# Optimization experiments

Measured on AMD Instinct MI355X. Metric: run time of the kernel, lower is better.

Reference implementation:

```python
import jax, jax.numpy as jnp
import numpy as np

HEAD_SIZE = 16
HIDDEN = 1024
NEG_INF = -1e9


def setup_inputs() -> dict:
    key = jax.random.key(0)
    ks = jax.random.split(key, 9)
    B, S, H = 2, 2048, HIDDEN
    q = jax.random.normal(ks[0], (B, S, H), dtype=jnp.float32)
    k = jax.random.normal(ks[1], (B, S, H), dtype=jnp.float32)
    v = jax.random.normal(ks[2], (B, S, H), dtype=jnp.float32)
    mask = jnp.ones((B, S), dtype=jnp.int32)
    scale = 1.0 / np.sqrt(H)
    wq = jax.random.normal(ks[3], (H, H), dtype=jnp.float32) * scale
    bq = jnp.zeros((H,), dtype=jnp.float32)
    wk = jax.random.normal(ks[4], (H, H), dtype=jnp.float32) * scale
    bk = jnp.zeros((H,), dtype=jnp.float32)
    wv = jax.random.normal(ks[5], (H, H), dtype=jnp.float32) * scale
    bv = jnp.zeros((H,), dtype=jnp.float32)
    return {"q": q, "k": k, "v": v, "mask": mask,
            "wq": wq, "bq": bq, "wk": wk, "bk": bk, "wv": wv, "bv": bv}


def _split_heads(x):
    # [B, S, H] -> [B, n_heads, S, head_dim]
    B, S, H = x.shape
    return x.reshape(B, S, HEAD_SIZE, H // HEAD_SIZE).transpose(0, 2, 1, 3)


def reference(q, k, v, mask, wq, bq, wk, bk, wv, bv):
    B, S, H = q.shape
    qh = _split_heads(q @ wq + bq)  # [B, nH, S, d]
    kh = _split_heads(k @ wk + bk)
    vh = _split_heads(v @ wv + bv)
    # scores scaled by sqrt(hidden_size) -- faithful to original (not head_dim)
    scores = jnp.einsum('bhqd,bhkd->bhqk', qh, kh) / jnp.sqrt(jnp.float32(H))
    # original: mask[0] of shape [B,S] -> [B,1,S,1], masks query rows
    m = mask.astype(jnp.float32)[:, None, :, None]  # [B,1,S,1]
    scores = scores + NEG_INF * (1.0 - m)
    weights = jax.nn.softmax(scores, axis=-1)
    out = jnp.einsum('bhqk,bhkd->bhqd', weights, vh)  # [B, nH, S, d]
    return out.transpose(0, 2, 1, 3).reshape(B, S, H)
```

## Files before the change

### kernel.cpp

```cpp
#include <hip/hip_runtime.h>
#include <hip/hip_bf16.h>
#include <math.h>

typedef __bf16 bf16_t;
typedef __bf16 bf16x8 __attribute__((ext_vector_type(8)));
typedef __bf16 bf16x4 __attribute__((ext_vector_type(4)));
typedef float floatx4 __attribute__((ext_vector_type(4)));

#define QSCALE 0.045084222f

__device__ __forceinline__ void gload_lds16(const bf16_t* g, bf16_t* l) {
  __builtin_amdgcn_global_load_lds(
      (const __attribute__((address_space(1))) void*)(g),
      (__attribute__((address_space(3))) void*)(l), 16, 0, 0);
}

__device__ __forceinline__ float fast_exp2(float x) {
  float r;
  asm("v_exp_f32 %0, %1" : "=v"(r) : "v"(x));
  return r;
}

__global__ __launch_bounds__(256) void cvt3_k(
    const float* __restrict__ q, const float* __restrict__ k,
    const float* __restrict__ v, bf16_t* __restrict__ xb) {
  const float* src = (blockIdx.y == 0) ? q : (blockIdx.y == 1) ? k : v;
  bf16_t* dst = xb + (size_t)blockIdx.y * 4194304u;
  const int i = (blockIdx.x * 256 + threadIdx.x) * 8;
  float4 f0 = *(const float4*)(src + i);
  float4 f1 = *(const float4*)(src + i + 4);
  bf16x8 hv;
  hv[0] = (bf16_t)f0.x; hv[1] = (bf16_t)f0.y;
  hv[2] = (bf16_t)f0.z; hv[3] = (bf16_t)f0.w;
  hv[4] = (bf16_t)f1.x; hv[5] = (bf16_t)f1.y;
  hv[6] = (bf16_t)f1.z; hv[7] = (bf16_t)f1.w;
  *(bf16x8*)(dst + i) = hv;
}

__global__ __launch_bounds__(256) void transpose3_k(
    const float* __restrict__ wq, const float* __restrict__ wk,
    const float* __restrict__ wv, bf16_t* __restrict__ wt) {
  __shared__ float tile[32][33];
  const float* src = (blockIdx.z == 0) ? wq : (blockIdx.z == 1) ? wk : wv;
  bf16_t* dst = wt + (size_t)blockIdx.z * (1024u * 1024u);
  const int tx = threadIdx.x, ty = threadIdx.y;
  const int x = blockIdx.x * 32 + tx;
  const int y = blockIdx.y * 32 + ty;
#pragma unroll
  for (int i = 0; i < 32; i += 8)
    tile[ty + i][tx] = src[(size_t)(y + i) * 1024 + x];
  __syncthreads();
  const int x2 = blockIdx.y * 32 + tx;
  const int y2 = blockIdx.x * 32 + ty;
#pragma unroll
  for (int i = 0; i < 32; i += 8)
    dst[(size_t)(y2 + i) * 1024 + x2] = (bf16_t)tile[tx][ty + i];
}

__global__ __launch_bounds__(256) void qkv_gemm_k(
    const bf16_t* __restrict__ xb3, const bf16_t* __restrict__ wt3,
    const float* __restrict__ bq, const float* __restrict__ bk,
    const float* __restrict__ bv, bf16_t* __restrict__ Qh,
    bf16_t* __restrict__ Kh, bf16_t* __restrict__ Vt) {
  const int proj = blockIdx.z;
  const bf16_t* X = xb3 + (size_t)proj * 4194304u;
  const bf16_t* Wt = wt3 + (size_t)proj * 1048576u;
  const float* bias = (proj == 0) ? bq : (proj == 1) ? bk : bv;

  __shared__ __align__(16) bf16_t As[128 * 64];
  __shared__ __align__(16) bf16_t Bs[128 * 64];

  const int t = threadIdx.x;
  const int lane = t & 63;
  const int w = t >> 6;
  const int wm = (w >> 1) * 64;
  const int wn = (w & 1) * 64;
  const int m0 = blockIdx.x * 128;
  const int n0 = blockIdx.y * 128;
  const int lm = lane & 15;
  const int lq = lane >> 4;

  int srow[4], sg[4];
#pragma unroll
  for (int c = 0; c < 4; ++c) {
    const int E = c * 2048 + t * 8;
    srow[c] = E >> 6;
    sg[c] = (((E >> 3) & 7) ^ (srow[c] & 7)) * 8;
  }

  floatx4 acc[4][4];
#pragma unroll
  for (int i = 0; i < 4; ++i)
#pragma unroll
    for (int j = 0; j < 4; ++j) acc[i][j] = (floatx4){0.f, 0.f, 0.f, 0.f};

  for (int k0 = 0; k0 < 1024; k0 += 64) {
    __syncthreads();
#pragma unroll
    for (int c = 0; c < 4; ++c) {
      const int E = c * 2048 + t * 8;
      gload_lds16(X + (size_t)(m0 + srow[c]) * 1024 + k0 + sg[c], As + E);
      gload_lds16(Wt + (size_t)(n0 + srow[c]) * 1024 + k0 + sg[c], Bs + E);
    }
    __syncthreads();

#pragma unroll
    for (int kc = 0; kc < 2; ++kc) {
      bf16x8 a[4], b[4];
#pragma unroll
      for (int i = 0; i < 4; ++i) {
        const int ch = ((kc * 4 + lq) ^ (lm & 7)) * 8;
        a[i] = *(const bf16x8*)(As + (wm + i * 16 + lm) * 64 + ch);
        b[i] = *(const bf16x8*)(Bs + (wn + i * 16 + lm) * 64 + ch);
      }
      if (proj < 2) {
#pragma unroll
        for (int i = 0; i < 4; ++i)
#pragma unroll
          for (int j = 0; j < 4; ++j)
            acc[i][j] = __builtin_amdgcn_mfma_f32_16x16x32_bf16(b[j], a[i],
                                                               acc[i][j], 0, 0, 0);
      } else {
#pragma unroll
        for (int i = 0; i < 4; ++i)
#pragma unroll
          for (int j = 0; j < 4; ++j)
            acc[i][j] = __builtin_amdgcn_mfma_f32_16x16x32_bf16(a[i], b[j],
                                                               acc[i][j], 0, 0, 0);
      }
    }
  }

  if (proj == 2) {
#pragma unroll
    for (int j = 0; j < 4; ++j) {
      const int gn = n0 + wn + j * 16 + lm;
      const float bval = bias[gn];
      const int h = gn >> 6, d = gn & 63;
#pragma unroll
      for (int i = 0; i < 4; ++i) {
        const int gm = m0 + wm + i * 16 + lq * 4;
        const int bb = gm >> 11, s0 = gm & 2047;
        bf16x4 pk;
#pragma unroll
        for (int ii = 0; ii < 4; ++ii) pk[ii] = (bf16_t)(acc[i][j][ii] + bval);
        *(bf16x4*)(Vt + (((size_t)bb * 16 + h) * 64 + d) * 2048 + s0) = pk;
      }
    }
  } else {
    bf16_t* outp = (proj == 0) ? Qh : Kh;
    const float scale = (proj == 0) ? QSCALE : 1.0f;
#pragma unroll
    for (int j = 0; j < 4; ++j) {
      const int nb = n0 + wn + j * 16 + lq * 4;
      float bs4[4];
#pragma unroll
      for (int ii = 0; ii < 4; ++ii) bs4[ii] = bias[nb + ii];
      const int h = nb >> 6, d0 = nb & 63;
#pragma unroll
      for (int i = 0; i < 4; ++i) {
        const int gm = m0 + wm + i * 16 + lm;
        const int bb = gm >> 11, s = gm & 2047;
        bf16x4 pk;
#pragma unroll
        for (int ii = 0; ii < 4; ++ii)
          pk[ii] = (bf16_t)((acc[i][j][ii] + bs4[ii]) * scale);
        *(bf16x4*)(outp + (((size_t)bb * 16 + h) * 2048 + s) * 64 + d0) = pk;
      }
    }
  }
}

__global__ __launch_bounds__(256) void attn_k(
    const bf16_t* __restrict__ Qh, const bf16_t* __restrict__ Kh,
    const bf16_t* __restrict__ Vt, float* __restrict__ out) {
  __shared__ __align__(16) bf16_t Ks[128 * 64];
  __shared__ __align__(16) bf16_t Vs[64 * 128];
  __shared__ __align__(16) bf16_t Ps[4][32 * 128];

  const int t = threadIdx.x;
  const int lane = t & 63;
  const int w = t >> 6;
  const int lm = lane & 15;
  const int lq = lane >> 4;
  const int b = blockIdx.x >> 4, h = blockIdx.x & 15;
  const int q0 = blockIdx.y * 128;
  const size_t bh = (size_t)b * 16 + h;
  const bf16_t* Qb = Qh + bh * (2048 * 64);
  const bf16_t* Kb = Kh + bh * (2048 * 64);
  const bf16_t* Vb = Vt + bh * (64 * 2048);

  bf16x8 qf[2][2];
#pragma unroll
  for (int im = 0; im < 2; ++im)
#pragma unroll
    for (int kc = 0; kc < 2; ++kc)
      qf[im][kc] = *(const bf16x8*)(Qb +
          (size_t)(q0 + w * 32 + im * 16 + lm) * 64 + kc * 32 + lq * 8);

  float lsum[2] = {0.f, 0.f};
  floatx4 accO[2][4];
#pragma unroll
  for (int im = 0; im < 2; ++im)
#pragma unroll
    for (int jd = 0; jd < 4; ++jd) accO[im][jd] = (floatx4){0.f, 0.f, 0.f, 0.f};

  bf16x8 kv[8];

#define LOAD_KV(kt)                                                          \
  {                                                                          \
    _Pragma("unroll") for (int c = 0; c < 4; ++c) {                          \
      const int e = c * 2048 + t * 8;                                        \
      const int key = e >> 6, gk = ((e >> 3) & 7) ^ (key & 7);               \
      kv[c] = *(const bf16x8*)(Kb + (size_t)((kt) + key) * 64 + gk * 8);     \
      const int vr = e >> 7, gv = ((e >> 3) & 15) ^ (vr & 15);               \
      kv[4 + c] = *(const bf16x8*)(Vb + (size_t)vr * 2048 + (kt) + gv * 8);  \
    }                                                                        \
  }

  LOAD_KV(0);

  for (int kt = 0; kt < 2048; kt += 128) {
    __syncthreads();
#pragma unroll
    for (int c = 0; c < 4; ++c) {
      const int e = c * 2048 + t * 8;
      *(bf16x8*)(Ks + e) = kv[c];
      *(bf16x8*)(Vs + e) = kv[4 + c];
    }
    __syncthreads();

    if (kt + 128 < 2048) LOAD_KV(kt + 128);

    floatx4 accS[2][8];
#pragma unroll
    for (int jn = 0; jn < 8; ++jn) {
      const int krow = jn * 16 + lm;
      const bf16x8 k0 = *(const bf16x8*)(Ks + krow * 64 + ((lq) ^ (lm & 7)) * 8);
      const bf16x8 k1 = *(const bf16x8*)(Ks + krow * 64 + ((4 + lq) ^ (lm & 7)) * 8);
#pragma unroll
      for (int im = 0; im < 2; ++im) {
        floatx4 z = {0.f, 0.f, 0.f, 0.f};
        z = __builtin_amdgcn_mfma_f32_16x16x32_bf16(k0, qf[im][0], z, 0, 0, 0);
        z = __builtin_amdgcn_mfma_f32_16x16x32_bf16(k1, qf[im][1], z, 0, 0, 0);
        accS[im][jn] = z;
      }
    }

#pragma unroll
    for (int im = 0; im < 2; ++im) {
      const int pr = im * 16 + lm;
#pragma unroll
      for (int jn = 0; jn < 8; ++jn) {
        bf16x4 pk;
#pragma unroll
        for (int ii = 0; ii < 4; ++ii) {
          const float p = fast_exp2(accS[im][jn][ii]);
          lsum[im] += p;
          pk[ii] = (bf16_t)p;
        }
        const int c2 = ((jn * 2) + (lq >> 1)) ^ lm;
        *(bf16x4*)(Ps[w] + pr * 128 + c2 * 8 + (lq & 1) * 4) = pk;
      }
    }
    asm volatile("s_waitcnt lgkmcnt(0)" ::: "memory");

#pragma unroll
    for (int kc = 0; kc < 4; ++kc) {
      bf16x8 ap[2];
#pragma unroll
      for (int im = 0; im < 2; ++im)
        ap[im] = *(const bf16x8*)(Ps[w] + (im * 16 + lm) * 128 +
                                  ((kc * 4 + lq) ^ lm) * 8);
#pragma unroll
      for (int jd = 0; jd < 4; ++jd) {
        const bf16x8 vf = *(const bf16x8*)(Vs + (jd * 16 + lm) * 128 +
                                           ((kc * 4 + lq) ^ lm) * 8);
#pragma unroll
        for (int im = 0; im < 2; ++im)
          accO[im][jd] =
              __builtin_amdgcn_mfma_f32_16x16x32_bf16(vf, ap[im], accO[im][jd], 0, 0, 0);
      }
    }
  }
#undef LOAD_KV

  float inv[2];
#pragma unroll
  for (int im = 0; im < 2; ++im) {
    float l = lsum[im];
    l += __shfl_xor(l, 16, 64);
    l += __shfl_xor(l, 32, 64);
    inv[im] = 1.0f / l;
  }

#pragma unroll
  for (int im = 0; im < 2; ++im) {
    const int s = q0 + w * 32 + im * 16 + lm;
    float* op = out + ((size_t)b * 2048 + s) * 1024 + h * 64 + lq * 4;
#pragma unroll
    for (int jd = 0; jd < 4; ++jd) {
      float4 o;
      o.x = accO[im][jd][0] * inv[im];
      o.y = accO[im][jd][1] * inv[im];
      o.z = accO[im][jd][2] * inv[im];
      o.w = accO[im][jd][3] * inv[im];
      *(float4*)(op + jd * 16) = o;
    }
  }
}

extern "C" void kernel_launch(void* const* d_in, const int* in_sizes, int n_in,
                              void* d_out, int out_size, void* d_ws, size_t ws_size,
                              hipStream_t stream) {
  (void)in_sizes; (void)n_in; (void)out_size; (void)ws_size;
  const float* q = (const float*)d_in[0];
  const float* k = (const float*)d_in[1];
  const float* v = (const float*)d_in[2];
  const float* wq = (const float*)d_in[4];
  const float* bq = (const float*)d_in[5];
  const float* wk = (const float*)d_in[6];
  const float* bk = (const float*)d_in[7];
  const float* wv = (const float*)d_in[8];
  const float* bv = (const float*)d_in[9];
  float* out = (float*)d_out;

  bf16_t* ws = (bf16_t*)d_ws;
  bf16_t* Xb = ws;
  bf16_t* Wt = ws + 12582912u;
  bf16_t* Qh = Wt + 3145728u;
  bf16_t* Kh = Qh + 4194304u;
  bf16_t* Vt = Kh + 4194304u;

  cvt3_k<<<dim3(2048, 3, 1), dim3(256, 1, 1), 0, stream>>>(q, k, v, Xb);
  transpose3_k<<<dim3(32, 32, 3), dim3(32, 8, 1), 0, stream>>>(wq, wk, wv, Wt);
  qkv_gemm_k<<<dim3(32, 8, 3), dim3(256, 1, 1), 0, stream>>>(
      Xb, Wt, bq, bk, bv, Qh, Kh, Vt);
  attn_k<<<dim3(32, 16, 1), dim3(256, 1, 1), 0, stream>>>(Qh, Kh, Vt, out);
}
```

Measured before the change: 203.5 us.

## Merge prep kernels, halve attention query tile, reuse K LDS for P, MFMA row sums

```diff
diff --git a/kernel.cpp b/kernel.cpp
--- a/kernel.cpp
+++ b/kernel.cpp
@@ -21,40 +21,42 @@
   return r;
 }
 
-__global__ __launch_bounds__(256) void cvt3_k(
+__global__ __launch_bounds__(256) void prep_k(
     const float* __restrict__ q, const float* __restrict__ k,
-    const float* __restrict__ v, bf16_t* __restrict__ xb) {
-  const float* src = (blockIdx.y == 0) ? q : (blockIdx.y == 1) ? k : v;
-  bf16_t* dst = xb + (size_t)blockIdx.y * 4194304u;
-  const int i = (blockIdx.x * 256 + threadIdx.x) * 8;
-  float4 f0 = *(const float4*)(src + i);
-  float4 f1 = *(const float4*)(src + i + 4);
-  bf16x8 hv;
-  hv[0] = (bf16_t)f0.x; hv[1] = (bf16_t)f0.y;
-  hv[2] = (bf16_t)f0.z; hv[3] = (bf16_t)f0.w;
-  hv[4] = (bf16_t)f1.x; hv[5] = (bf16_t)f1.y;
-  hv[6] = (bf16_t)f1.z; hv[7] = (bf16_t)f1.w;
-  *(bf16x8*)(dst + i) = hv;
-}
-
-__global__ __launch_bounds__(256) void transpose3_k(
-    const float* __restrict__ wq, const float* __restrict__ wk,
-    const float* __restrict__ wv, bf16_t* __restrict__ wt) {
-  __shared__ float tile[32][33];
-  const float* src = (blockIdx.z == 0) ? wq : (blockIdx.z == 1) ? wk : wv;
-  bf16_t* dst = wt + (size_t)blockIdx.z * (1024u * 1024u);
-  const int tx = threadIdx.x, ty = threadIdx.y;
-  const int x = blockIdx.x * 32 + tx;
-  const int y = blockIdx.y * 32 + ty;
-#pragma unroll
-  for (int i = 0; i < 32; i += 8)
-    tile[ty + i][tx] = src[(size_t)(y + i) * 1024 + x];
-  __syncthreads();
-  const int x2 = blockIdx.y * 32 + tx;
-  const int y2 = blockIdx.x * 32 + ty;
-#pragma unroll
-  for (int i = 0; i < 32; i += 8)
-    dst[(size_t)(y2 + i) * 1024 + x2] = (bf16_t)tile[tx][ty + i];
+    const float* __restrict__ v, const float* __restrict__ wq,
+    const float* __restrict__ wk, const float* __restrict__ wv,
+    bf16_t* __restrict__ xb, bf16_t* __restrict__ wt) {
+  const int z = blockIdx.y;
+  const int t = threadIdx.x;
+  if (blockIdx.x < 2048) {
+    const float* src = (z == 0) ? q : (z == 1) ? k : v;
+    bf16_t* dst = xb + (size_t)z * 4194304u;
+    const int i = (blockIdx.x * 256 + t) * 8;
+    float4 f0 = *(const float4*)(src + i);
+    float4 f1 = *(const float4*)(src + i + 4);
+    bf16x8 hv;
+    hv[0] = (bf16_t)f0.x; hv[1] = (bf16_t)f0.y;
+    hv[2] = (bf16_t)f0.z; hv[3] = (bf16_t)f0.w;
+    hv[4] = (bf16_t)f1.x; hv[5] = (bf16_t)f1.y;
+    hv[6] = (bf16_t)f1.z; hv[7] = (bf16_t)f1.w;
+    *(bf16x8*)(dst + i) = hv;
+  } else {
+    __shared__ float tile[32][33];
+    const int bi = blockIdx.x - 2048;
+    const int bx = bi & 31, by = bi >> 5;
+    const float* src = (z == 0) ? wq : (z == 1) ? wk : wv;
+    bf16_t* dst = wt + (size_t)z * 1048576u;
+    const int tx = t & 31, ty = t >> 5;
+    const int x = bx * 32 + tx, y = by * 32 + ty;
+#pragma unroll
+    for (int i = 0; i < 32; i += 8)
+      tile[ty + i][tx] = src[(size_t)(y + i) * 1024 + x];
+    __syncthreads();
+    const int x2 = by * 32 + tx, y2 = bx * 32 + ty;
+#pragma unroll
+    for (int i = 0; i < 32; i += 8)
+      dst[(size_t)(y2 + i) * 1024 + x2] = (bf16_t)tile[tx][ty + i];
+  }
 }
 
 __global__ __launch_bounds__(256) void qkv_gemm_k(
@@ -176,7 +178,6 @@
     const bf16_t* __restrict__ Vt, float* __restrict__ out) {
   __shared__ __align__(16) bf16_t Ks[128 * 64];
   __shared__ __align__(16) bf16_t Vs[64 * 128];
-  __shared__ __align__(16) bf16_t Ps[4][32 * 128];
 
   const int t = threadIdx.x;
   const int lane = t & 63;
@@ -184,26 +185,27 @@
   const int lm = lane & 15;
   const int lq = lane >> 4;
   const int b = blockIdx.x >> 4, h = blockIdx.x & 15;
-  const int q0 = blockIdx.y * 128;
+  const int q0 = blockIdx.y * 64;
   const size_t bh = (size_t)b * 16 + h;
   const bf16_t* Qb = Qh + bh * (2048 * 64);
   const bf16_t* Kb = Kh + bh * (2048 * 64);
   const bf16_t* Vb = Vt + bh * (64 * 2048);
-
-  bf16x8 qf[2][2];
-#pragma unroll
-  for (int im = 0; im < 2; ++im)
-#pragma unroll
-    for (int kc = 0; kc < 2; ++kc)
-      qf[im][kc] = *(const bf16x8*)(Qb +
-          (size_t)(q0 + w * 32 + im * 16 + lm) * 64 + kc * 32 + lq * 8);
-
-  float lsum[2] = {0.f, 0.f};
-  floatx4 accO[2][4];
-#pragma unroll
-  for (int im = 0; im < 2; ++im)
-#pragma unroll
-    for (int jd = 0; jd < 4; ++jd) accO[im][jd] = (floatx4){0.f, 0.f, 0.f, 0.f};
+  bf16_t* Pw = Ks + w * 2048;
+
+  bf16x8 qf[2];
+#pragma unroll
+  for (int kc = 0; kc < 2; ++kc)
+    qf[kc] = *(const bf16x8*)(Qb + (size_t)(q0 + w * 16 + lm) * 64 + kc * 32 +
+                              lq * 8);
+
+  bf16x8 ones;
+#pragma unroll
+  for (int j = 0; j < 8; ++j) ones[j] = (bf16_t)1.0f;
+
+  floatx4 accO[4], accL;
+#pragma unroll
+  for (int jd = 0; jd < 4; ++jd) accO[jd] = (floatx4){0.f, 0.f, 0.f, 0.f};
+  accL = (floatx4){0.f, 0.f, 0.f, 0.f};
 
   bf16x8 kv[8];
 
@@ -232,81 +234,57 @@
 
     if (kt + 128 < 2048) LOAD_KV(kt + 128);
 
-    floatx4 accS[2][8];
+    floatx4 accS[8];
 #pragma unroll
     for (int jn = 0; jn < 8; ++jn) {
       const int krow = jn * 16 + lm;
       const bf16x8 k0 = *(const bf16x8*)(Ks + krow * 64 + ((lq) ^ (lm & 7)) * 8);
       const bf16x8 k1 = *(const bf16x8*)(Ks + krow * 64 + ((4 + lq) ^ (lm & 7)) * 8);
-#pragma unroll
-      for (int im = 0; im < 2; ++im) {
-        floatx4 z = {0.f, 0.f, 0.f, 0.f};
-        z = __builtin_amdgcn_mfma_f32_16x16x32_bf16(k0, qf[im][0], z, 0, 0, 0);
-        z = __builtin_amdgcn_mfma_f32_16x16x32_bf16(k1, qf[im][1], z, 0, 0, 0);
-        accS[im][jn] = z;
-      }
-    }
-
-#pragma unroll
-    for (int im = 0; im < 2; ++im) {
-      const int pr = im * 16 + lm;
-#pragma unroll
-      for (int jn = 0; jn < 8; ++jn) {
-        bf16x4 pk;
-#pragma unroll
-        for (int ii = 0; ii < 4; ++ii) {
-          const float p = fast_exp2(accS[im][jn][ii]);
-          lsum[im] += p;
-          pk[ii] = (bf16_t)p;
-        }
-        const int c2 = ((jn * 2) + (lq >> 1)) ^ lm;
-        *(bf16x4*)(Ps[w] + pr * 128 + c2 * 8 + (lq & 1) * 4) = pk;
-      }
+      floatx4 z = {0.f, 0.f, 0.f, 0.f};
+      z = __builtin_amdgcn_mfma_f32_16x16x32_bf16(k0, qf[0], z, 0, 0, 0);
+      z = __builtin_amdgcn_mfma_f32_16x16x32_bf16(k1, qf[1], z, 0, 0, 0);
+      accS[jn] = z;
+    }
+
+    __syncthreads();
+
+#pragma unroll
+    for (int jn = 0; jn < 8; ++jn) {
+      bf16x4 pk;
+#pragma unroll
+      for (int ii = 0; ii < 4; ++ii) pk[ii] = (bf16_t)fast_exp2(accS[jn][ii]);
+      const int c2 = ((jn * 2) + (lq >> 1)) ^ lm;
+      *(bf16x4*)(Pw + lm * 128 + c2 * 8 + (lq & 1) * 4) = pk;
     }
     asm volatile("s_waitcnt lgkmcnt(0)" ::: "memory");
 
 #pragma unroll
     for (int kc = 0; kc < 4; ++kc) {
-      bf16x8 ap[2];
-#pragma unroll
-      for (int im = 0; im < 2; ++im)
-        ap[im] = *(const bf16x8*)(Ps[w] + (im * 16 + lm) * 128 +
-                                  ((kc * 4 + lq) ^ lm) * 8);
+      const bf16x8 ap =
+          *(const bf16x8*)(Pw + lm * 128 + ((kc * 4 + lq) ^ lm) * 8);
 #pragma unroll
       for (int jd = 0; jd < 4; ++jd) {
         const bf16x8 vf = *(const bf16x8*)(Vs + (jd * 16 + lm) * 128 +
                                            ((kc * 4 + lq) ^ lm) * 8);
-#pragma unroll
-        for (int im = 0; im < 2; ++im)
-          accO[im][jd] =
-              __builtin_amdgcn_mfma_f32_16x16x32_bf16(vf, ap[im], accO[im][jd], 0, 0, 0);
-      }
+        accO[jd] = __builtin_amdgcn_mfma_f32_16x16x32_bf16(vf, ap, accO[jd], 0, 0, 0);
+      }
+      accL = __builtin_amdgcn_mfma_f32_16x16x32_bf16(ones, ap, accL, 0, 0, 0);
     }
   }
 #undef LOAD_KV
 
-  float inv[2];
-#pragma unroll
-  for (int im = 0; im < 2; ++im) {
-    float l = lsum[im];
-    l += __shfl_xor(l, 16, 64);
-    l += __shfl_xor(l, 32, 64);
-    inv[im] = 1.0f / l;
-  }
-
-#pragma unroll
-  for (int im = 0; im < 2; ++im) {
-    const int s = q0 + w * 32 + im * 16 + lm;
-    float* op = out + ((size_t)b * 2048 + s) * 1024 + h * 64 + lq * 4;
-#pragma unroll
-    for (int jd = 0; jd < 4; ++jd) {
-      float4 o;
-      o.x = accO[im][jd][0] * inv[im];
-      o.y = accO[im][jd][1] * inv[im];
-      o.z = accO[im][jd][2] * inv[im];
-      o.w = accO[im][jd][3] * inv[im];
-      *(float4*)(op + jd * 16) = o;
-    }
+  const float inv = 1.0f / accL[0];
+
+  const int s = q0 + w * 16 + lm;
+  float* op = out + ((size_t)b * 2048 + s) * 1024 + h * 64 + lq * 4;
+#pragma unroll
+  for (int jd = 0; jd < 4; ++jd) {
+    float4 o;
+    o.x = accO[jd][0] * inv;
+    o.y = accO[jd][1] * inv;
+    o.z = accO[jd][2] * inv;
+    o.w = accO[jd][3] * inv;
+    *(float4*)(op + jd * 16) = o;
   }
 }
 
@@ -332,9 +310,9 @@
   bf16_t* Kh = Qh + 4194304u;
   bf16_t* Vt = Kh + 4194304u;
 
-  cvt3_k<<<dim3(2048, 3, 1), dim3(256, 1, 1), 0, stream>>>(q, k, v, Xb);
-  transpose3_k<<<dim3(32, 32, 3), dim3(32, 8, 1), 0, stream>>>(wq, wk, wv, Wt);
+  prep_k<<<dim3(3072, 3, 1), dim3(256, 1, 1), 0, stream>>>(
+      q, k, v, wq, wk, wv, Xb, Wt);
   qkv_gemm_k<<<dim3(32, 8, 3), dim3(256, 1, 1), 0, stream>>>(
       Xb, Wt, bq, bk, bv, Qh, Kh, Vt);
-  attn_k<<<dim3(32, 16, 1), dim3(256, 1, 1), 0, stream>>>(Qh, Kh, Vt, out);
-}
+  attn_k<<<dim3(32, 32, 1), dim3(256, 1, 1), 0, stream>>>(Qh, Kh, Vt, out);
+}
```

After: 203.8 us. Within noise of the previous version (+0.2%).
